# Performance work log

Hardware: AMD Instinct MI355X
Metric: run time of the kernel (lower is better)

Reference implementation:

```python
import jax, jax.numpy as jnp
import numpy as np

N_NODES = 100000
N_EDGES = 1600000
N_PAIRS = 200000
IN_CH = 128
HID_CH = 128


def _graph_conv(x, src, dst, edge_weight, w_rel, b_rel, w_root, num_nodes):
    # PyG GraphConv with aggr='mean':
    # out = lin_rel(mean_{j in N(i)}(x_j * w_ij)) + lin_root(x_i)
    msg = x[src] * edge_weight[:, None]                       # [E, C] gather
    agg = jax.ops.segment_sum(msg, dst, num_segments=num_nodes)  # [N, C]
    cnt = jax.ops.segment_sum(jnp.ones((src.shape[0],), x.dtype), dst,
                              num_segments=num_nodes)          # in-degree
    agg = agg / jnp.maximum(cnt, 1.0)[:, None]                 # mean aggr
    return agg @ w_rel + b_rel + x @ w_root


def setup_inputs() -> dict:
    key = jax.random.key(0)
    ks = jax.random.split(key, 10)
    x = jax.random.normal(ks[0], (N_NODES, IN_CH), dtype=jnp.float32)
    edge_index = jax.random.randint(ks[1], (2, N_EDGES), 0, N_NODES, dtype=jnp.int32)
    edge_weight = jax.random.uniform(ks[2], (N_EDGES,), dtype=jnp.float32)
    edge_label_index = jax.random.randint(ks[3], (2, N_PAIRS), 0, N_NODES, dtype=jnp.int32)
    s1 = 1.0 / np.sqrt(IN_CH)
    s2 = 1.0 / np.sqrt(HID_CH)
    w1_rel = jax.random.uniform(ks[4], (IN_CH, HID_CH), jnp.float32, -s1, s1)
    b1_rel = jnp.zeros((HID_CH,), jnp.float32)
    w1_root = jax.random.uniform(ks[5], (IN_CH, HID_CH), jnp.float32, -s1, s1)
    w2_rel = jax.random.uniform(ks[6], (HID_CH, HID_CH), jnp.float32, -s2, s2)
    b2_rel = jnp.zeros((HID_CH,), jnp.float32)
    w2_root = jax.random.uniform(ks[7], (HID_CH, HID_CH), jnp.float32, -s2, s2)
    return {"x": x, "edge_index": edge_index, "edge_weight": edge_weight,
            "edge_label_index": edge_label_index,
            "w1_rel": w1_rel, "b1_rel": b1_rel, "w1_root": w1_root,
            "w2_rel": w2_rel, "b2_rel": b2_rel, "w2_root": w2_root}


def reference(x, edge_index, edge_weight, edge_label_index,
              w1_rel, b1_rel, w1_root, w2_rel, b2_rel, w2_root):
    src, dst = edge_index[0], edge_index[1]
    # encode
    h = _graph_conv(x, src, dst, edge_weight, w1_rel, b1_rel, w1_root, x.shape[0])
    h = jax.nn.relu(h)
    z = _graph_conv(h, src, dst, edge_weight, w2_rel, b2_rel, w2_root, x.shape[0])
    # decode: scaled dot product between candidate pair embeddings
    zs = z[edge_label_index[0]]   # [P, H]
    zd = z[edge_label_index[1]]   # [P, H]
    scale = z.shape[-1] ** 0.5
    return jnp.sum(zs * zd, axis=-1) / scale
```

## Files before the change

kernel.cpp:

```cpp
#include <hip/hip_runtime.h>

#define NN 100000
#define NE 1600000
#define NP 200000
#define CH 128
#define SB 1024
#define LK 264

typedef _Float16 f16x8 __attribute__((ext_vector_type(8)));
typedef _Float16 f16x4 __attribute__((ext_vector_type(4)));
typedef _Float16 f16x2 __attribute__((ext_vector_type(2)));
typedef float f32x4 __attribute__((ext_vector_type(4)));

__global__ void cast_kernel(const float* __restrict__ in, _Float16* __restrict__ out, int n8) {
    int i = blockIdx.x * blockDim.x + threadIdx.x;
    if (i >= n8) return;
    const float4* p = (const float4*)in + (size_t)i * 2;
    float4 a = p[0], b = p[1];
    f16x8 o = { (_Float16)a.x, (_Float16)a.y, (_Float16)a.z, (_Float16)a.w,
                (_Float16)b.x, (_Float16)b.y, (_Float16)b.z, (_Float16)b.w };
    *((f16x8*)out + i) = o;
}

__global__ void count_rank_kernel(const int* __restrict__ dst, int* __restrict__ cnt,
                                  int* __restrict__ rank, int E) {
    int e = blockIdx.x * blockDim.x + threadIdx.x;
    if (e < E) rank[e] = atomicAdd(&cnt[dst[e]], 1);
}

__global__ __launch_bounds__(SB)
void scan1_kernel(const int* __restrict__ cnt, int* __restrict__ row_ptr,
                  int* __restrict__ partials, int n) {
    __shared__ int s[SB];
    int i = blockIdx.x * SB + threadIdx.x;
    int v = (i < n) ? cnt[i] : 0;
    s[threadIdx.x] = v;
    __syncthreads();
    for (int off = 1; off < SB; off <<= 1) {
        int t = (threadIdx.x >= off) ? s[threadIdx.x - off] : 0;
        __syncthreads();
        s[threadIdx.x] += t;
        __syncthreads();
    }
    if (i < n) row_ptr[i + 1] = s[threadIdx.x];
    if (threadIdx.x == SB - 1) partials[blockIdx.x] = s[SB - 1];
}

__global__ __launch_bounds__(128)
void scan2_kernel(int* __restrict__ partials, int nb) {
    __shared__ int s[128];
    int v = (threadIdx.x < nb) ? partials[threadIdx.x] : 0;
    s[threadIdx.x] = v;
    __syncthreads();
    for (int off = 1; off < 128; off <<= 1) {
        int t = (threadIdx.x >= off) ? s[threadIdx.x - off] : 0;
        __syncthreads();
        s[threadIdx.x] += t;
        __syncthreads();
    }
    if (threadIdx.x < nb) partials[threadIdx.x] = s[threadIdx.x];
}

__global__ __launch_bounds__(SB)
void scan3_kernel(int* __restrict__ row_ptr, const int* __restrict__ partials, int n) {
    int i = blockIdx.x * SB + threadIdx.x;
    if (i < n && blockIdx.x > 0) row_ptr[i + 1] += partials[blockIdx.x - 1];
    if (i == 0) row_ptr[0] = 0;
}

__global__ void fill_kernel(const int* __restrict__ src, const int* __restrict__ dst,
                            const float* __restrict__ ew, const int* __restrict__ row_ptr,
                            const int* __restrict__ rank, int2* __restrict__ csr, int E) {
    int e = blockIdx.x * blockDim.x + threadIdx.x;
    if (e >= E) return;
    int pos = row_ptr[dst[e]] + rank[e];
    csr[pos] = make_int2(src[e], __float_as_int(ew[e]));
}

__global__ __launch_bounds__(256)
void gather_kernel(const _Float16* __restrict__ feat, const int* __restrict__ row_ptr,
                   const int2* __restrict__ csr, _Float16* __restrict__ agg, int N) {
    int node = blockIdx.x * 4 + (threadIdx.x >> 6);
    if (node >= N) return;
    int lane = threadIdx.x & 63;
    int q = lane >> 4;
    int l16 = lane & 15;
    int c8 = l16 << 3;
    int r0 = row_ptr[node], r1 = row_ptr[node + 1];
    float acc[8] = {0.f, 0.f, 0.f, 0.f, 0.f, 0.f, 0.f, 0.f};
    for (int r = r0 + q; r < r1; r += 4) {
        int2 e = csr[r];
        float w = __int_as_float(e.y);
        f16x8 v = *(const f16x8*)&feat[(size_t)e.x * CH + c8];
#pragma unroll
        for (int j = 0; j < 8; j++) acc[j] += w * (float)v[j];
    }
#pragma unroll
    for (int j = 0; j < 8; j++) {
        acc[j] += __shfl_xor(acc[j], 16, 64);
        acc[j] += __shfl_xor(acc[j], 32, 64);
    }
    if (q == 0) {
        float inv = 1.0f / fmaxf((float)(r1 - r0), 1.0f);
        f16x8 o;
#pragma unroll
        for (int j = 0; j < 8; j++) o[j] = (_Float16)(acc[j] * inv);
        *(f16x8*)&agg[(size_t)node * CH + c8] = o;
    }
}

__global__ void prep_w_kernel(const float* __restrict__ wr, const float* __restrict__ wo,
                              _Float16* __restrict__ wt) {
    int idx = blockIdx.x * 256 + threadIdx.x;
    if (idx >= 128 * 256) return;
    int n = idx >> 8, k = idx & 255;
    float v = (k < 128) ? wr[k * 128 + n] : wo[(k - 128) * 128 + n];
    wt[idx] = (_Float16)v;
}

template <bool RELU>
__global__ __launch_bounds__(256)
void layer_mfma_kernel(const _Float16* __restrict__ agg,
                       const _Float16* __restrict__ xin,
                       const _Float16* __restrict__ wt,
                       const float* __restrict__ bias,
                       _Float16* __restrict__ out, int N) {
    __shared__ _Float16 s_a[64][LK];

    const int tid = threadIdx.x;
    const int nb = blockIdx.x * 64;

    for (int i = tid; i < 64 * 32; i += 256) {
        int r = i >> 5;
        int c8 = (i & 31) << 3;
        int gn = nb + r;
        f16x8 v = {};
        if (gn < N) {
            const _Float16* srcp = (c8 < 128) ? &agg[(size_t)gn * CH + c8]
                                              : &xin[(size_t)gn * CH + (c8 - 128)];
            v = *(const f16x8*)srcp;
        }
        *(f16x8*)&s_a[r][c8] = v;
    }
    __syncthreads();

    const int wave = tid >> 6;
    const int lane = tid & 63;
    const int quad = lane >> 4;
    const int l16  = lane & 15;

    f32x4 acc[4][2];
#pragma unroll
    for (int m = 0; m < 4; m++)
#pragma unroll
        for (int t = 0; t < 2; t++) acc[m][t] = (f32x4){0.f, 0.f, 0.f, 0.f};

    const int kq = quad * 8;

#pragma unroll
    for (int ks = 0; ks < 8; ks++) {
        int kbase = ks * 32 + kq;
        f16x8 bf[2];
#pragma unroll
        for (int t = 0; t < 2; t++) {
            int n = wave * 32 + t * 16 + l16;
            bf[t] = *(const f16x8*)&wt[(size_t)n * 256 + kbase];
        }
#pragma unroll
        for (int m = 0; m < 4; m++) {
            f16x8 af = *(const f16x8*)&s_a[m * 16 + l16][kbase];
            acc[m][0] = __builtin_amdgcn_mfma_f32_16x16x32_f16(af, bf[0], acc[m][0], 0, 0, 0);
            acc[m][1] = __builtin_amdgcn_mfma_f32_16x16x32_f16(af, bf[1], acc[m][1], 0, 0, 0);
        }
    }

    float bv[2];
    bv[0] = bias[wave * 32 + l16];
    bv[1] = bias[wave * 32 + 16 + l16];

#pragma unroll
    for (int m = 0; m < 4; m++) {
#pragma unroll
        for (int r = 0; r < 4; r++) {
            int node = nb + m * 16 + quad * 4 + r;
            if (node >= N) continue;
#pragma unroll
            for (int t = 0; t < 2; t++) {
                float v = acc[m][t][r] + bv[t];
                if (RELU) v = fmaxf(v, 0.f);
                out[(size_t)node * CH + wave * 32 + t * 16 + l16] = (_Float16)v;
            }
        }
    }
}

__global__ void decode_kernel(const _Float16* __restrict__ z,
                              const int* __restrict__ ps,
                              const int* __restrict__ pd,
                              float* __restrict__ out, int P) {
    long tid = (long)blockIdx.x * blockDim.x + threadIdx.x;
    int p = (int)(tid >> 6);
    int lane = (int)(tid & 63);
    if (p >= P) return;
    int s = ps[p], d = pd[p];
    f16x2 a = *(const f16x2*)&z[(size_t)s * CH + lane * 2];
    f16x2 b = *(const f16x2*)&z[(size_t)d * CH + lane * 2];
    float v = (float)a[0] * (float)b[0] + (float)a[1] * (float)b[1];
#pragma unroll
    for (int off = 32; off > 0; off >>= 1) v += __shfl_down(v, off, 64);
    if (lane == 0) out[p] = v * 0.08838834764831845f;
}

extern "C" void kernel_launch(void* const* d_in, const int* in_sizes, int n_in,
                              void* d_out, int out_size, void* d_ws, size_t ws_size,
                              hipStream_t stream) {
    const float* x       = (const float*)d_in[0];
    const int*   ei      = (const int*)d_in[1];
    const float* ew      = (const float*)d_in[2];
    const int*   eli     = (const int*)d_in[3];
    const float* w1_rel  = (const float*)d_in[4];
    const float* b1      = (const float*)d_in[5];
    const float* w1_root = (const float*)d_in[6];
    const float* w2_rel  = (const float*)d_in[7];
    const float* b2      = (const float*)d_in[8];
    const float* w2_root = (const float*)d_in[9];
    float* out = (float*)d_out;

    const int N = NN, E = NE, P = NP;
    const size_t hrow = (size_t)N * CH * sizeof(_Float16);

    char* ws = (char*)d_ws;
    _Float16* xh   = (_Float16*)(ws);
    _Float16* aggh = (_Float16*)(ws + hrow);
    _Float16* hh   = (_Float16*)(ws + 2 * hrow);
    _Float16* zh   = aggh;
    size_t off = 3 * hrow;
    int* cnt      = (int*)(ws + off); off += (size_t)N * 4;
    int* row_ptr  = (int*)(ws + off); off += (size_t)(N + 1) * 4;
    int* partials = (int*)(ws + off); off += 256 * 4;
    int* rank     = (int*)(ws + off); off += (size_t)E * 4;
    off = (off + 15) & ~(size_t)15;
    int2* csr     = (int2*)(ws + off); off += (size_t)E * 8;
    _Float16* w1t = (_Float16*)(ws + off); off += (size_t)128 * 256 * 2;
    _Float16* w2t = (_Float16*)(ws + off); off += (size_t)128 * 256 * 2;

    const int* src = ei;
    const int* dst = ei + E;

    const int nb_scan = (N + SB - 1) / SB;
    const int n8 = N * CH / 8;

    cast_kernel<<<(n8 + 255) / 256, 256, 0, stream>>>(x, xh, n8);
    prep_w_kernel<<<128, 256, 0, stream>>>(w1_rel, w1_root, w1t);
    prep_w_kernel<<<128, 256, 0, stream>>>(w2_rel, w2_root, w2t);

    hipMemsetAsync(cnt, 0, (size_t)N * 4, stream);
    count_rank_kernel<<<(E + 255) / 256, 256, 0, stream>>>(dst, cnt, rank, E);
    scan1_kernel<<<nb_scan, SB, 0, stream>>>(cnt, row_ptr, partials, N);
    scan2_kernel<<<1, 128, 0, stream>>>(partials, nb_scan);
    scan3_kernel<<<nb_scan, SB, 0, stream>>>(row_ptr, partials, N);
    fill_kernel<<<(E + 255) / 256, 256, 0, stream>>>(src, dst, ew, row_ptr, rank, csr, E);

    gather_kernel<<<(N + 3) / 4, 256, 0, stream>>>(xh, row_ptr, csr, aggh, N);
    layer_mfma_kernel<true><<<(N + 63) / 64, 256, 0, stream>>>(aggh, xh, w1t, b1, hh, N);

    gather_kernel<<<(N + 3) / 4, 256, 0, stream>>>(hh, row_ptr, csr, aggh, N);
    layer_mfma_kernel<false><<<(N + 63) / 64, 256, 0, stream>>>(aggh, hh, w2t, b2, zh, N);

    {
        long threads = (long)P * 64;
        decode_kernel<<<(int)((threads + 255) / 256), 256, 0, stream>>>(zh, eli, eli + P, out, P);
    }
}
```

Baseline: 448.4 us.

## Pad degree counters, batch atomics per thread, software-pipeline gather loads

Each degree counter now sits on its own 64-byte slot, so atomic increments to neighbouring nodes no longer contend on the same cache line. Each thread of count_rank now handles eight edges with vectorized loads and stores. The gather loop is software-pipelined so the next edge's CSR entry and feature row are loaded before the current one is accumulated, hiding memory latency. In exchange the counter array is sixteen times larger, so the memset is bigger and scan1 reads counters with a strided pattern.

```diff
diff --git a/kernel.cpp b/kernel.cpp
--- a/kernel.cpp
+++ b/kernel.cpp
@@ -6,9 +6,9 @@
 #define CH 128
 #define SB 1024
 #define LK 264
+#define CPAD 16
 
 typedef _Float16 f16x8 __attribute__((ext_vector_type(8)));
-typedef _Float16 f16x4 __attribute__((ext_vector_type(4)));
 typedef _Float16 f16x2 __attribute__((ext_vector_type(2)));
 typedef float f32x4 __attribute__((ext_vector_type(4)));
 
@@ -24,8 +24,22 @@
 
 __global__ void count_rank_kernel(const int* __restrict__ dst, int* __restrict__ cnt,
                                   int* __restrict__ rank, int E) {
-    int e = blockIdx.x * blockDim.x + threadIdx.x;
-    if (e < E) rank[e] = atomicAdd(&cnt[dst[e]], 1);
+    int t = blockIdx.x * blockDim.x + threadIdx.x;
+    int e0 = t * 8;
+    if (e0 >= E) return;
+    int4 d0 = *(const int4*)&dst[e0];
+    int4 d1 = *(const int4*)&dst[e0 + 4];
+    int4 r0, r1;
+    r0.x = atomicAdd(&cnt[d0.x * CPAD], 1);
+    r0.y = atomicAdd(&cnt[d0.y * CPAD], 1);
+    r0.z = atomicAdd(&cnt[d0.z * CPAD], 1);
+    r0.w = atomicAdd(&cnt[d0.w * CPAD], 1);
+    r1.x = atomicAdd(&cnt[d1.x * CPAD], 1);
+    r1.y = atomicAdd(&cnt[d1.y * CPAD], 1);
+    r1.z = atomicAdd(&cnt[d1.z * CPAD], 1);
+    r1.w = atomicAdd(&cnt[d1.w * CPAD], 1);
+    *(int4*)&rank[e0] = r0;
+    *(int4*)&rank[e0 + 4] = r1;
 }
 
 __global__ __launch_bounds__(SB)
@@ -33,7 +47,7 @@
                   int* __restrict__ partials, int n) {
     __shared__ int s[SB];
     int i = blockIdx.x * SB + threadIdx.x;
-    int v = (i < n) ? cnt[i] : 0;
+    int v = (i < n) ? cnt[i * CPAD] : 0;
     s[threadIdx.x] = v;
     __syncthreads();
     for (int off = 1; off < SB; off <<= 1) {
@@ -88,10 +102,19 @@
     int c8 = l16 << 3;
     int r0 = row_ptr[node], r1 = row_ptr[node + 1];
     float acc[8] = {0.f, 0.f, 0.f, 0.f, 0.f, 0.f, 0.f, 0.f};
-    for (int r = r0 + q; r < r1; r += 4) {
+    int r = r0 + q;
+    if (r < r1) {
         int2 e = csr[r];
+        f16x8 v = *(const f16x8*)&feat[(size_t)e.x * CH + c8];
+        for (r += 4; r < r1; r += 4) {
+            int2 e2 = csr[r];
+            f16x8 v2 = *(const f16x8*)&feat[(size_t)e2.x * CH + c8];
+            float w = __int_as_float(e.y);
+#pragma unroll
+            for (int j = 0; j < 8; j++) acc[j] += w * (float)v[j];
+            e = e2; v = v2;
+        }
         float w = __int_as_float(e.y);
-        f16x8 v = *(const f16x8*)&feat[(size_t)e.x * CH + c8];
 #pragma unroll
         for (int j = 0; j < 8; j++) acc[j] += w * (float)v[j];
     }
@@ -230,19 +253,19 @@
     const size_t hrow = (size_t)N * CH * sizeof(_Float16);
 
     char* ws = (char*)d_ws;
-    _Float16* xh   = (_Float16*)(ws);
-    _Float16* aggh = (_Float16*)(ws + hrow);
-    _Float16* hh   = (_Float16*)(ws + 2 * hrow);
+    size_t off = 0;
+    auto alloc = [&](size_t bytes) { char* p = ws + off; off = (off + bytes + 15) & ~(size_t)15; return p; };
+    _Float16* xh   = (_Float16*)alloc(hrow);
+    _Float16* aggh = (_Float16*)alloc(hrow);
+    _Float16* hh   = (_Float16*)alloc(hrow);
     _Float16* zh   = aggh;
-    size_t off = 3 * hrow;
-    int* cnt      = (int*)(ws + off); off += (size_t)N * 4;
-    int* row_ptr  = (int*)(ws + off); off += (size_t)(N + 1) * 4;
-    int* partials = (int*)(ws + off); off += 256 * 4;
-    int* rank     = (int*)(ws + off); off += (size_t)E * 4;
-    off = (off + 15) & ~(size_t)15;
-    int2* csr     = (int2*)(ws + off); off += (size_t)E * 8;
-    _Float16* w1t = (_Float16*)(ws + off); off += (size_t)128 * 256 * 2;
-    _Float16* w2t = (_Float16*)(ws + off); off += (size_t)128 * 256 * 2;
+    int* cnt      = (int*)alloc((size_t)N * CPAD * 4);
+    int* row_ptr  = (int*)alloc((size_t)(N + 1) * 4);
+    int* partials = (int*)alloc(256 * 4);
+    int* rank     = (int*)alloc((size_t)E * 4);
+    int2* csr     = (int2*)alloc((size_t)E * 8);
+    _Float16* w1t = (_Float16*)alloc((size_t)128 * 256 * 2);
+    _Float16* w2t = (_Float16*)alloc((size_t)128 * 256 * 2);
 
     const int* src = ei;
     const int* dst = ei + E;
@@ -254,8 +277,11 @@
     prep_w_kernel<<<128, 256, 0, stream>>>(w1_rel, w1_root, w1t);
     prep_w_kernel<<<128, 256, 0, stream>>>(w2_rel, w2_root, w2t);
 
-    hipMemsetAsync(cnt, 0, (size_t)N * 4, stream);
-    count_rank_kernel<<<(E + 255) / 256, 256, 0, stream>>>(dst, cnt, rank, E);
+    hipMemsetAsync(cnt, 0, (size_t)N * CPAD * 4, stream);
+    {
+        int nthr = E / 8;
+        count_rank_kernel<<<(nthr + 255) / 256, 256, 0, stream>>>(dst, cnt, rank, E);
+    }
     scan1_kernel<<<nb_scan, SB, 0, stream>>>(cnt, row_ptr, partials, N);
     scan2_kernel<<<1, 128, 0, stream>>>(partials, nb_scan);
     scan3_kernel<<<nb_scan, SB, 0, stream>>>(row_ptr, partials, N);
```

Result: no change. 439.8 us (-1.9%).
